# Kernel optimization log

Measured on AMD Instinct MI355X. Metric: run time of the kernel, lower is better.

The kernel has to match this reference:

```python
import jax, jax.numpy as jnp
import numpy as np

GROUP = 64  # group_size for precision='int4'


def setup_inputs() -> dict:
    key = jax.random.key(0)
    ks = jax.random.split(key, 7)
    B, S, C, O, R = 64, 4, 8192, 8192, 32
    x = jax.random.normal(ks[0], (B, S, C), dtype=jnp.float32)
    # unpacked int4 weight values stored as int32 codes in [0,16) -> value = code - 8
    qweight = jax.random.randint(ks[1], (O, C), 0, 16, dtype=jnp.int32)
    wscales = jax.random.uniform(ks[2], (C // GROUP, O), dtype=jnp.float32,
                                 minval=0.005, maxval=0.02)
    # smoothing factors kept strictly positive and away from zero
    smooth_factor = jax.random.uniform(ks[3], (C,), dtype=jnp.float32,
                                       minval=0.5, maxval=1.5)
    proj_down = jax.random.normal(ks[4], (C, R), dtype=jnp.float32) * 0.02
    proj_up = jax.random.normal(ks[5], (O, R), dtype=jnp.float32) * 0.02
    bias = jax.random.normal(ks[6], (O,), dtype=jnp.float32) * 0.01
    return {"x": x, "qweight": qweight, "wscales": wscales,
            "smooth_factor": smooth_factor, "proj_down": proj_down,
            "proj_up": proj_up, "bias": bias}


def reference(x, qweight, wscales, smooth_factor, proj_down, proj_up, bias):
    B, S, C = x.shape
    O = qweight.shape[0]
    ng = C // GROUP
    xr = x.reshape(B * S, C)

    # SVD low-rank correction: lora_act = x @ proj_down ; out += lora_act @ proj_up^T
    lora = (xr @ proj_down) @ proj_up.T  # (M, O)

    # activation smoothing + per-group symmetric int4 quantization
    xs = xr / smooth_factor                                   # (M, C)
    xg = xs.reshape(-1, ng, GROUP)                            # (M, ng, 64)
    ascales = jnp.max(jnp.abs(xg), axis=-1, keepdims=True) / 7.0
    ascales = jnp.maximum(ascales, 1e-8)
    q_act = jnp.clip(jnp.round(xg / ascales), -8.0, 7.0)
    x_deq = (q_act * ascales).reshape(-1, C)                  # dequantized act

    # per-group weight dequant: wscales is (ng, O)
    w = (qweight.astype(jnp.float32) - 8.0).reshape(O, ng, GROUP)
    w_deq = (w * wscales.T[:, :, None]).reshape(O, C)         # (O, C)

    out = x_deq @ w_deq.T + lora + bias                       # (M, O)
    return out.reshape(B, S, O)
```

## Files before the change

kernel.cpp:

```cpp
#include <hip/hip_runtime.h>
#include <stdint.h>

#define C_DIM 8192
#define O_DIM 8192
#define M_DIM 256
#define NG    128
#define RK    32

typedef float f32x4 __attribute__((ext_vector_type(4)));
typedef int   i32x4 __attribute__((ext_vector_type(4)));
typedef unsigned int u32;

__device__ __forceinline__ void gll16(const void* g, void* l) {
  __builtin_amdgcn_global_load_lds(
      (const __attribute__((address_space(1))) void*)g,
      (__attribute__((address_space(3))) void*)l, 16, 0, 0);
}

__global__ __launch_bounds__(256) void k_lora(const float* __restrict__ x,
                                              const float* __restrict__ pd,
                                              float* __restrict__ lact) {
  const int t  = threadIdx.x;
  const int rq = t & 7;
  const int kc = (t >> 3) & 15;
  const int ml = t >> 7;
  const int m  = blockIdx.x * 2 + ml;
  const float* xrow = x + (size_t)m * C_DIM + kc * 512;
  const float* pdp  = pd + (size_t)(kc * 512) * RK + rq * 4;
  float a0 = 0.f, a1 = 0.f, a2 = 0.f, a3 = 0.f;
  for (int k = 0; k < 512; k += 4) {
    float4 xv = *(const float4*)(xrow + k);
    float4 p0 = *(const float4*)(pdp + (size_t)(k + 0) * RK);
    float4 p1 = *(const float4*)(pdp + (size_t)(k + 1) * RK);
    float4 p2 = *(const float4*)(pdp + (size_t)(k + 2) * RK);
    float4 p3 = *(const float4*)(pdp + (size_t)(k + 3) * RK);
    a0 += xv.x * p0.x + xv.y * p1.x + xv.z * p2.x + xv.w * p3.x;
    a1 += xv.x * p0.y + xv.y * p1.y + xv.z * p2.y + xv.w * p3.y;
    a2 += xv.x * p0.z + xv.y * p1.z + xv.z * p2.z + xv.w * p3.z;
    a3 += xv.x * p0.w + xv.y * p1.w + xv.z * p2.w + xv.w * p3.w;
  }
  __shared__ float red[2][8][16][4];
  red[ml][rq][kc][0] = a0;
  red[ml][rq][kc][1] = a1;
  red[ml][rq][kc][2] = a2;
  red[ml][rq][kc][3] = a3;
  __syncthreads();
  if (t < 64) {
    const int ml2 = t >> 5, r = t & 31, rq2 = r >> 2, j = r & 3;
    float s = 0.f;
#pragma unroll
    for (int c = 0; c < 16; ++c) s += red[ml2][rq2][c][j];
    lact[(size_t)(blockIdx.x * 2 + ml2) * RK + r] = s;
  }
}

__global__ __launch_bounds__(256) void k_prep(const float* __restrict__ x,
                                              const float* __restrict__ smooth,
                                              float* __restrict__ scp,
                                              i32x4* __restrict__ wsA8) {
  const int t    = threadIdx.x;
  const int ml   = t & 15;
  const int gl   = t >> 4;
  const int MT   = blockIdx.x >> 3;
  const int gblk = blockIdx.x & 7;
  const int m = MT * 16 + ml;
  const int g = gblk * 16 + gl;
  const float* xp = x + (size_t)m * C_DIM + g * 64;
  const float* sp = smooth + g * 64;
  float xs[64];
  float amax = 0.0f;
#pragma unroll
  for (int i = 0; i < 64; i += 4) {
    float4 xv = *(const float4*)(xp + i);
    float4 sv = *(const float4*)(sp + i);
    xs[i + 0] = xv.x / sv.x;
    xs[i + 1] = xv.y / sv.y;
    xs[i + 2] = xv.z / sv.z;
    xs[i + 3] = xv.w / sv.w;
    amax = fmaxf(amax, fabsf(xs[i + 0]));
    amax = fmaxf(amax, fabsf(xs[i + 1]));
    amax = fmaxf(amax, fabsf(xs[i + 2]));
    amax = fmaxf(amax, fabsf(xs[i + 3]));
  }
  const float ascale = fmaxf(amax / 7.0f, 1e-8f);
  int qi[64];
  int rs = 0;
#pragma unroll
  for (int i = 0; i < 64; ++i) {
    float qv = fminf(fmaxf(rintf(xs[i] / ascale), -8.0f), 7.0f);
    qi[i] = (int)qv;
    rs += qi[i];
  }
  scp[(size_t)g * 512 + m]       = ascale;
  scp[(size_t)g * 512 + 256 + m] = 8.0f * (float)rs * ascale;
  const size_t base = ((size_t)(MT * NG + g)) * 64;
#pragma unroll
  for (int lg = 0; lg < 4; ++lg) {
    const int* q = qi + lg * 16;
    i32x4 c;
#pragma unroll
    for (int dw = 0; dw < 4; ++dw)
      c[dw] = (q[dw * 4 + 0] & 0xff) | ((q[dw * 4 + 1] & 0xff) << 8) |
              ((q[dw * 4 + 2] & 0xff) << 16) | (q[dw * 4 + 3] << 24);
    wsA8[base + lg * 16 + ml] = c;
  }
}

__global__ __launch_bounds__(256, 2) void k_main(
    const int* __restrict__ qw, const float* __restrict__ wsc,
    const float* __restrict__ pu, const float* __restrict__ bias,
    const float* __restrict__ scp, const i32x4* __restrict__ wsA8,
    const float* __restrict__ lact, float* __restrict__ out) {
  const int t    = threadIdx.x;
  const int n0   = blockIdx.x * 16;
  const int w    = t >> 6;
  const int l    = t & 63;
  const int lrow = l >> 4;
  const int lcol = l & 15;
  const int MTb  = w * 4;

  __shared__ int   ldsB[4][1024];
  __shared__ float ldsSC[2][1024];
  __shared__ float ldsW[NG * 16];

  for (int i = t; i < NG * 16; i += 256) {
    int g = i >> 4, c = i & 15;
    ldsW[i] = wsc[(size_t)g * O_DIM + n0 + c];
  }

  const int sr     = t >> 4;
  const int scp_   = t & 15;
  const int schunk = scp_ ^ (sr & 7);
  const int*   gB  = qw + (size_t)(n0 + sr) * C_DIM + schunk * 4;
  const float* gSC = scp + t * 4;

  __syncthreads();

  gll16(gB, &ldsB[0][t * 4]);
  gll16(gSC, &ldsSC[0][t * 4]);
  i32x4 A0[4], A1[4];
#pragma unroll
  for (int mi = 0; mi < 4; ++mi)
    A0[mi] = wsA8[((size_t)(MTb + mi) * NG + 0) * 64 + l];
  gll16(gB + 64, &ldsB[1][t * 4]);

  f32x4 acc[4];
#pragma unroll
  for (int mi = 0; mi < 4; ++mi) acc[mi] = (f32x4){0.f, 0.f, 0.f, 0.f};

  const i32x4 z = (i32x4){0, 0, 0, 0};
  const int rsw = (lcol & 7);

#define BODY(G, AC, AN, VMC, DO_SC)                                            \
  {                                                                            \
    asm volatile("s_waitcnt vmcnt(" #VMC ")" ::: "memory");                    \
    __builtin_amdgcn_s_barrier();                                              \
    const int bb = (G) & 3;                                                    \
    i32x4 raw0 = *(const i32x4*)&ldsB[bb][lcol * 64 + ((lrow * 4 + 0) ^ rsw) * 4]; \
    i32x4 raw1 = *(const i32x4*)&ldsB[bb][lcol * 64 + ((lrow * 4 + 1) ^ rsw) * 4]; \
    i32x4 raw2 = *(const i32x4*)&ldsB[bb][lcol * 64 + ((lrow * 4 + 2) ^ rsw) * 4]; \
    i32x4 raw3 = *(const i32x4*)&ldsB[bb][lcol * 64 + ((lrow * 4 + 3) ^ rsw) * 4]; \
    i32x4 bf;                                                                  \
    bf[0] = raw0[0] | (raw0[1] << 8) | (raw0[2] << 16) | (raw0[3] << 24);      \
    bf[1] = raw1[0] | (raw1[1] << 8) | (raw1[2] << 16) | (raw1[3] << 24);      \
    bf[2] = raw2[0] | (raw2[1] << 8) | (raw2[2] << 16) | (raw2[3] << 24);      \
    bf[3] = raw3[0] | (raw3[1] << 8) | (raw3[2] << 16) | (raw3[3] << 24);      \
                \
    {                                                                          \
      int gn = (G) + 1; if (gn > NG - 1) gn = NG - 1;                          \
      _Pragma("unroll")                                                        \
      for (int mi = 0; mi < 4; ++mi)                                           \
        AN[mi] = wsA8[((size_t)(MTb + mi) * NG + gn) * 64 + l];                \
    }                                                                          \
    if (DO_SC) {                                                               \
      int pn = ((G) >> 1) + 1; if (pn > 63) pn = 63;                           \
      gll16(gSC + (size_t)pn * 1024, &ldsSC[pn & 1][t * 4]);                   \
    }                                                                          \
    {                                                                          \
      int gs = (G) + 2; if (gs > NG - 1) gs = NG - 1;                          \
      gll16(gB + (size_t)gs * 64, &ldsB[gs & 3][t * 4]);                       \
    }                                                                          \
    const int sb = ((G) >> 1) & 1;                                             \
    const int gh = ((G) & 1) * 512;                                            \
    const float wsv = ldsW[(G) * 16 + lcol];                                   \
    _Pragma("unroll")                                                          \
    for (int mi = 0; mi < 4; ++mi) {                                           \
      f32x4 asv = *(const f32x4*)&ldsSC[sb][gh + (MTb + mi) * 16 + lrow * 4];  \
      f32x4 rsv = *(const f32x4*)&ldsSC[sb][gh + 256 + (MTb + mi) * 16 + lrow * 4]; \
      i32x4 d = __builtin_amdgcn_mfma_i32_16x16x64_i8(AC[mi], bf, z, 0, 0, 0); \
      f32x4 df;                                                                \
      df[0] = (float)d[0]; df[1] = (float)d[1];                                \
      df[2] = (float)d[2]; df[3] = (float)d[3];                                \
      acc[mi] += wsv * (asv * df - rsv);                                       \
    }                                                                          \
  }

  for (int p = 0; p < NG / 2; ++p) {
    const int g0 = p * 2;
    BODY(g0, A0, A1, 1, 1);
    BODY(g0 + 1, A1, A0, 2, 0);
  }
#undef BODY

  const int n = n0 + lcol;
  const float bv = bias[n];
  float4 puq[8];
#pragma unroll
  for (int rq = 0; rq < 8; ++rq)
    puq[rq] = *(const float4*)(pu + (size_t)n * RK + rq * 4);
#pragma unroll
  for (int mi = 0; mi < 4; ++mi) {
#pragma unroll
    for (int j = 0; j < 4; ++j) {
      const int m = (MTb + mi) * 16 + lrow * 4 + j;
      const float* lp = lact + (size_t)m * RK;
      float lo = 0.f;
#pragma unroll
      for (int rq = 0; rq < 8; ++rq) {
        float4 lv = *(const float4*)(lp + rq * 4);
        lo += lv.x * puq[rq].x + lv.y * puq[rq].y + lv.z * puq[rq].z +
              lv.w * puq[rq].w;
      }
      out[(size_t)m * O_DIM + n] = acc[mi][j] + bv + lo;
    }
  }
}

extern "C" void kernel_launch(void* const* d_in, const int* in_sizes, int n_in,
                              void* d_out, int out_size, void* d_ws,
                              size_t ws_size, hipStream_t stream) {
  const float* x      = (const float*)d_in[0];
  const int*   qw     = (const int*)d_in[1];
  const float* wsc    = (const float*)d_in[2];
  const float* smooth = (const float*)d_in[3];
  const float* pd     = (const float*)d_in[4];
  const float* pu     = (const float*)d_in[5];
  const float* bias   = (const float*)d_in[6];
  float* out = (float*)d_out;

  char* ws = (char*)d_ws;
  float* lact = (float*)ws;
  float* scp  = (float*)(ws + 32 * 1024);
  i32x4* wsA8 = (i32x4*)(ws + 288 * 1024);

  hipLaunchKernelGGL(k_prep, dim3(128), dim3(256), 0, stream, x, smooth, scp,
                     wsA8);
  hipLaunchKernelGGL(k_lora, dim3(128), dim3(256), 0, stream, x, pd, lact);
  hipLaunchKernelGGL(k_main, dim3(512), dim3(256), 0, stream, qw, wsc, pu, bias,
                     scp, wsA8, lact, out);
}
```

Measured before the change: 181.6 us.

## Split M across two blocks, pack weights into LDS, deepen prefetch pipeline

The main kernel now launches twice as many blocks, each handling half of the M rows (two 16-row tiles per wave instead of four). The activation scale layout is reshaped to match. Weight codes are loaded into registers and packed to int8 before being written to a swizzled LDS buffer, instead of being copied raw via global_load_lds and packed after the LDS read. The prefetch distance grows to three groups, and occupancy is raised to four blocks per CU. The intent is more parallelism and occupancy and less LDS traffic per MFMA, at the cost of re-reading each weight tile in both M halves and taking an extra LDS write and wait every step.

```diff
diff --git a/kernel.cpp b/kernel.cpp
--- a/kernel.cpp
+++ b/kernel.cpp
@@ -11,10 +11,10 @@
 typedef int   i32x4 __attribute__((ext_vector_type(4)));
 typedef unsigned int u32;
 
-__device__ __forceinline__ void gll16(const void* g, void* l) {
+__device__ __forceinline__ void gll4(const void* g, void* l) {
   __builtin_amdgcn_global_load_lds(
       (const __attribute__((address_space(1))) void*)g,
-      (__attribute__((address_space(3))) void*)l, 16, 0, 0);
+      (__attribute__((address_space(3))) void*)l, 4, 0, 0);
 }
 
 __global__ __launch_bounds__(256) void k_lora(const float* __restrict__ x,
@@ -56,7 +56,7 @@
 
 __global__ __launch_bounds__(256) void k_prep(const float* __restrict__ x,
                                               const float* __restrict__ smooth,
-                                              float* __restrict__ scp,
+                                              float* __restrict__ scp3,
                                               i32x4* __restrict__ wsA8) {
   const int t    = threadIdx.x;
   const int ml   = t & 15;
@@ -91,8 +91,9 @@
     qi[i] = (int)qv;
     rs += qi[i];
   }
-  scp[(size_t)g * 512 + m]       = ascale;
-  scp[(size_t)g * 512 + 256 + m] = 8.0f * (float)rs * ascale;
+  const int h = m >> 7, mll = m & 127;
+  scp3[((size_t)h * NG + g) * 256 + mll]       = ascale;
+  scp3[((size_t)h * NG + g) * 256 + 128 + mll] = 8.0f * (float)rs * ascale;
   const size_t base = ((size_t)(MT * NG + g)) * 64;
 #pragma unroll
   for (int lg = 0; lg < 4; ++lg) {
@@ -106,99 +107,101 @@
   }
 }
 
-__global__ __launch_bounds__(256, 2) void k_main(
+__global__ __launch_bounds__(256, 4) void k_main(
     const int* __restrict__ qw, const float* __restrict__ wsc,
     const float* __restrict__ pu, const float* __restrict__ bias,
-    const float* __restrict__ scp, const i32x4* __restrict__ wsA8,
+    const float* __restrict__ scp3, const i32x4* __restrict__ wsA8,
     const float* __restrict__ lact, float* __restrict__ out) {
   const int t    = threadIdx.x;
-  const int n0   = blockIdx.x * 16;
+  const int bid  = blockIdx.x;
+  const int mh   = bid & 1;
+  const int n0   = (bid >> 1) * 16;
   const int w    = t >> 6;
   const int l    = t & 63;
   const int lrow = l >> 4;
   const int lcol = l & 15;
-  const int MTb  = w * 4;
-
-  __shared__ int   ldsB[4][1024];
-  __shared__ float ldsSC[2][1024];
+
+  __shared__ int   ldsBf[4 * 256];
+  __shared__ float ldsSCf[4 * 256];
   __shared__ float ldsW[NG * 16];
 
-  for (int i = t; i < NG * 16; i += 256) {
-    int g = i >> 4, c = i & 15;
-    ldsW[i] = wsc[(size_t)g * O_DIM + n0 + c];
-  }
-
-  const int sr     = t >> 4;
-  const int scp_   = t & 15;
-  const int schunk = scp_ ^ (sr & 7);
-  const int*   gB  = qw + (size_t)(n0 + sr) * C_DIM + schunk * 4;
-  const float* gSC = scp + t * 4;
+  for (int i = t; i < NG * 16; i += 256)
+    ldsW[i] = wsc[(size_t)(i >> 4) * O_DIM + n0 + (i & 15)];
+
+  const int sr = t >> 4, cg = t & 15;
+  const int* gB = qw + (size_t)(n0 + sr) * C_DIM + cg * 4;
+  const int pwIdx = sr * 16 + (((cg >> 2) ^ ((sr >> 1) & 3)) << 2) + (cg & 3);
+  const int rdIdx = lcol * 16 + ((lrow ^ ((lcol >> 1) & 3)) << 2);
+
+  const float* gSC = scp3 + ((size_t)mh * NG) * 256 + t;
+  const i32x4* gA0 = wsA8 + ((size_t)(mh * 8 + w * 2 + 0) * NG) * 64 + l;
+  const i32x4* gA1 = wsA8 + ((size_t)(mh * 8 + w * 2 + 1) * NG) * 64 + l;
+
+  const int scBase = w * 32 + lrow * 4;
 
   __syncthreads();
 
-  gll16(gB, &ldsB[0][t * 4]);
-  gll16(gSC, &ldsSC[0][t * 4]);
-  i32x4 A0[4], A1[4];
-#pragma unroll
-  for (int mi = 0; mi < 4; ++mi)
-    A0[mi] = wsA8[((size_t)(MTb + mi) * NG + 0) * 64 + l];
-  gll16(gB + 64, &ldsB[1][t * 4]);
-
-  f32x4 acc[4];
-#pragma unroll
-  for (int mi = 0; mi < 4; ++mi) acc[mi] = (f32x4){0.f, 0.f, 0.f, 0.f};
-
+  i32x4 bR0, bR1, bR2, bR3;
+  i32x4 A0_0, A0_1, A1_0, A1_1, A2_0, A2_1, A3_0, A3_1;
+
+  bR0 = *(const i32x4*)(gB);
+  gll4(gSC, &ldsSCf[0 * 256 + t]);
+  A0_0 = gA0[0];
+  A0_1 = gA1[0];
+  asm volatile("" ::: "memory");
+  bR1 = *(const i32x4*)(gB + 64);
+  gll4(gSC + 256, &ldsSCf[1 * 256 + t]);
+  A1_0 = gA0[64];
+  A1_1 = gA1[64];
+  asm volatile("" ::: "memory");
+  bR2 = *(const i32x4*)(gB + 128);
+  gll4(gSC + 512, &ldsSCf[2 * 256 + t]);
+  A2_0 = gA0[128];
+  A2_1 = gA1[128];
+
+  f32x4 acc0 = (f32x4){0.f, 0.f, 0.f, 0.f};
+  f32x4 acc1 = (f32x4){0.f, 0.f, 0.f, 0.f};
   const i32x4 z = (i32x4){0, 0, 0, 0};
-  const int rsw = (lcol & 7);
-
-#define BODY(G, AC, AN, VMC, DO_SC)                                            \
+
+#define BODY(U, UP3, G)                                                        \
   {                                                                            \
-    asm volatile("s_waitcnt vmcnt(" #VMC ")" ::: "memory");                    \
+    asm volatile("s_waitcnt vmcnt(8) lgkmcnt(0)" ::: "memory");                \
+    int pk = (bR##U[0] & 0xff) | ((bR##U[1] & 0xff) << 8) |                    \
+             ((bR##U[2] & 0xff) << 16) | (bR##U[3] << 24);                     \
+    ldsBf[(U) * 256 + pwIdx] = pk;                                             \
+    asm volatile("s_waitcnt lgkmcnt(0)" ::: "memory");                         \
     __builtin_amdgcn_s_barrier();                                              \
-    const int bb = (G) & 3;                                                    \
-    i32x4 raw0 = *(const i32x4*)&ldsB[bb][lcol * 64 + ((lrow * 4 + 0) ^ rsw) * 4]; \
-    i32x4 raw1 = *(const i32x4*)&ldsB[bb][lcol * 64 + ((lrow * 4 + 1) ^ rsw) * 4]; \
-    i32x4 raw2 = *(const i32x4*)&ldsB[bb][lcol * 64 + ((lrow * 4 + 2) ^ rsw) * 4]; \
-    i32x4 raw3 = *(const i32x4*)&ldsB[bb][lcol * 64 + ((lrow * 4 + 3) ^ rsw) * 4]; \
-    i32x4 bf;                                                                  \
-    bf[0] = raw0[0] | (raw0[1] << 8) | (raw0[2] << 16) | (raw0[3] << 24);      \
-    bf[1] = raw1[0] | (raw1[1] << 8) | (raw1[2] << 16) | (raw1[3] << 24);      \
-    bf[2] = raw2[0] | (raw2[1] << 8) | (raw2[2] << 16) | (raw2[3] << 24);      \
-    bf[3] = raw3[0] | (raw3[1] << 8) | (raw3[2] << 16) | (raw3[3] << 24);      \
-                \
+    i32x4 bf = *(const i32x4*)&ldsBf[(U) * 256 + rdIdx];                       \
+    f32x4 as0 = *(const f32x4*)&ldsSCf[(U) * 256 + scBase];                    \
+    f32x4 rs0 = *(const f32x4*)&ldsSCf[(U) * 256 + scBase + 128];              \
+    f32x4 as1 = *(const f32x4*)&ldsSCf[(U) * 256 + scBase + 16];               \
+    f32x4 rs1 = *(const f32x4*)&ldsSCf[(U) * 256 + scBase + 144];              \
+    const float wsv = ldsW[(G) * 16 + lcol];                                   \
     {                                                                          \
-      int gn = (G) + 1; if (gn > NG - 1) gn = NG - 1;                          \
-      _Pragma("unroll")                                                        \
-      for (int mi = 0; mi < 4; ++mi)                                           \
-        AN[mi] = wsA8[((size_t)(MTb + mi) * NG + gn) * 64 + l];                \
+      int g3 = (G) + 3;                                                        \
+      if (g3 > NG - 1) g3 = NG - 1;                                            \
+      bR##UP3 = *(const i32x4*)(gB + (size_t)g3 * 64);                         \
+      gll4(gSC + (size_t)g3 * 256, &ldsSCf[(UP3) * 256 + t]);                  \
+      A##UP3##_0 = gA0[(size_t)g3 * 64];                                       \
+      A##UP3##_1 = gA1[(size_t)g3 * 64];                                       \
     }                                                                          \
-    if (DO_SC) {                                                               \
-      int pn = ((G) >> 1) + 1; if (pn > 63) pn = 63;                           \
-      gll16(gSC + (size_t)pn * 1024, &ldsSC[pn & 1][t * 4]);                   \
-    }                                                                          \
-    {                                                                          \
-      int gs = (G) + 2; if (gs > NG - 1) gs = NG - 1;                          \
-      gll16(gB + (size_t)gs * 64, &ldsB[gs & 3][t * 4]);                       \
-    }                                                                          \
-    const int sb = ((G) >> 1) & 1;                                             \
-    const int gh = ((G) & 1) * 512;                                            \
-    const float wsv = ldsW[(G) * 16 + lcol];                                   \
-    _Pragma("unroll")                                                          \
-    for (int mi = 0; mi < 4; ++mi) {                                           \
-      f32x4 asv = *(const f32x4*)&ldsSC[sb][gh + (MTb + mi) * 16 + lrow * 4];  \
-      f32x4 rsv = *(const f32x4*)&ldsSC[sb][gh + 256 + (MTb + mi) * 16 + lrow * 4]; \
-      i32x4 d = __builtin_amdgcn_mfma_i32_16x16x64_i8(AC[mi], bf, z, 0, 0, 0); \
-      f32x4 df;                                                                \
-      df[0] = (float)d[0]; df[1] = (float)d[1];                                \
-      df[2] = (float)d[2]; df[3] = (float)d[3];                                \
-      acc[mi] += wsv * (asv * df - rsv);                                       \
-    }                                                                          \
-  }
-
-  for (int p = 0; p < NG / 2; ++p) {
-    const int g0 = p * 2;
-    BODY(g0, A0, A1, 1, 1);
-    BODY(g0 + 1, A1, A0, 2, 0);
+    i32x4 d0 = __builtin_amdgcn_mfma_i32_16x16x64_i8(A##U##_0, bf, z, 0, 0, 0);\
+    i32x4 d1 = __builtin_amdgcn_mfma_i32_16x16x64_i8(A##U##_1, bf, z, 0, 0, 0);\
+    f32x4 df0, df1;                                                            \
+    df0[0] = (float)d0[0]; df0[1] = (float)d0[1];                              \
+    df0[2] = (float)d0[2]; df0[3] = (float)d0[3];                              \
+    df1[0] = (float)d1[0]; df1[1] = (float)d1[1];                              \
+    df1[2] = (float)d1[2]; df1[3] = (float)d1[3];                              \
+    acc0 += wsv * (as0 * df0 - rs0);                                           \
+    acc1 += wsv * (as1 * df1 - rs1);                                           \
+  }
+
+  for (int p = 0; p < NG / 4; ++p) {
+    const int g0 = p * 4;
+    BODY(0, 3, g0 + 0)
+    BODY(1, 0, g0 + 1)
+    BODY(2, 1, g0 + 2)
+    BODY(3, 2, g0 + 3)
   }
 #undef BODY
 
@@ -209,10 +212,11 @@
   for (int rq = 0; rq < 8; ++rq)
     puq[rq] = *(const float4*)(pu + (size_t)n * RK + rq * 4);
 #pragma unroll
-  for (int mi = 0; mi < 4; ++mi) {
+  for (int mi = 0; mi < 2; ++mi) {
+    const f32x4 av = (mi == 0) ? acc0 : acc1;
 #pragma unroll
     for (int j = 0; j < 4; ++j) {
-      const int m = (MTb + mi) * 16 + lrow * 4 + j;
+      const int m = mh * 128 + (w * 2 + mi) * 16 + lrow * 4 + j;
       const float* lp = lact + (size_t)m * RK;
       float lo = 0.f;
 #pragma unroll
@@ -221,7 +225,7 @@
         lo += lv.x * puq[rq].x + lv.y * puq[rq].y + lv.z * puq[rq].z +
               lv.w * puq[rq].w;
       }
-      out[(size_t)m * O_DIM + n] = acc[mi][j] + bv + lo;
+      out[(size_t)m * O_DIM + n] = av[j] + bv + lo;
     }
   }
 }
@@ -240,12 +244,12 @@
 
   char* ws = (char*)d_ws;
   float* lact = (float*)ws;
-  float* scp  = (float*)(ws + 32 * 1024);
+  float* scp3 = (float*)(ws + 32 * 1024);
   i32x4* wsA8 = (i32x4*)(ws + 288 * 1024);
 
-  hipLaunchKernelGGL(k_prep, dim3(128), dim3(256), 0, stream, x, smooth, scp,
+  hipLaunchKernelGGL(k_prep, dim3(128), dim3(256), 0, stream, x, smooth, scp3,
                      wsA8);
   hipLaunchKernelGGL(k_lora, dim3(128), dim3(256), 0, stream, x, pd, lact);
-  hipLaunchKernelGGL(k_main, dim3(512), dim3(256), 0, stream, qw, wsc, pu, bias,
-                     scp, wsA8, lact, out);
-}
+  hipLaunchKernelGGL(k_main, dim3(1024), dim3(256), 0, stream, qw, wsc, pu,
+                     bias, scp3, wsA8, lact, out);
+}
```

Measured after the change: 192.0 us. 1.06x slower.
